# Kernel optimization log

Measured on AMD Instinct MI355X. Metric: run time of the kernel, lower is better.

The kernel has to match this reference:

```python
import jax, jax.numpy as jnp
import numpy as np

D_IN = 1024
D_OUT = 1024
SEQ = 2048
BATCH = 4


def setup_inputs() -> dict:
    key = jax.random.key(0)
    k_x, k_q, k_k, k_v = jax.random.split(key, 4)
    scale = 1.0 / np.sqrt(D_IN)  # ~ torch Linear init scale
    x = jax.random.normal(k_x, (BATCH, SEQ, D_IN), dtype=jnp.float32)
    # torch nn.Linear weights have shape [d_out, d_in]; y = x @ W.T
    Wq = jax.random.uniform(k_q, (D_OUT, D_IN), jnp.float32, -scale, scale)
    Wk = jax.random.uniform(k_k, (D_OUT, D_IN), jnp.float32, -scale, scale)
    Wv = jax.random.uniform(k_v, (D_OUT, D_IN), jnp.float32, -scale, scale)
    return {"x": x, "Wq": Wq, "Wk": Wk, "Wv": Wv}


def reference(x, Wq, Wk, Wv):
    # projections (no bias, qkv_bias=False)
    q = jnp.einsum("bsd,ed->bse", x, Wq)  # [B,S,D_OUT]
    k = jnp.einsum("bsd,ed->bse", x, Wk)
    v = jnp.einsum("bsd,ed->bse", x, Wv)
    scores = jnp.einsum("bqe,bke->bqk", q, k)  # [B,S,S]
    seq = scores.shape[-1]
    causal = jnp.tril(jnp.ones((seq, seq), dtype=bool))  # keep lower-tri
    scores = jnp.where(causal[None], scores, -jnp.inf)
    # note: original scales AFTER masking: softmax(scores / sqrt(d_k))
    inv_sqrt_dk = 1.0 / np.sqrt(k.shape[-1]).astype(np.float32)
    weights = jax.nn.softmax(scores * inv_sqrt_dk, axis=-1)
    # dropout p=0.0 (eval-equivalent): identity
    return jnp.einsum("bqk,bke->bqe", weights, v)
```

## Files before the change

### kernel.cpp

```cpp
#include <hip/hip_runtime.h>
#include <hip/hip_bf16.h>

typedef __bf16 v8bf __attribute__((ext_vector_type(8)));
typedef float v4f __attribute__((ext_vector_type(4)));

#define GBL_AS(p) ((const __attribute__((address_space(1))) unsigned int*)(p))
#define LDS_AS(p) ((__attribute__((address_space(3))) unsigned int*)(p))

__global__ void cast_f32_bf16(const float* __restrict__ src,
                              __hip_bfloat16* __restrict__ dst, int n) {
  int i = (blockIdx.x * 256 + threadIdx.x) * 4;
  if (i >= n) return;
  float4 f = *(const float4*)(src + i);
  union { __hip_bfloat16 h[4]; uint2 u; } pk;
  pk.h[0] = __float2bfloat16(f.x);
  pk.h[1] = __float2bfloat16(f.y);
  pk.h[2] = __float2bfloat16(f.z);
  pk.h[3] = __float2bfloat16(f.w);
  *(uint2*)(dst + i) = pk.u;
}

__global__ void cast_w3(const float* __restrict__ a, const float* __restrict__ b,
                        const float* __restrict__ c, __hip_bfloat16* __restrict__ dst) {
  int seg = blockIdx.x >> 10;
  const float* src = seg == 0 ? a : (seg == 1 ? b : c);
  int i = ((blockIdx.x & 1023) * 256 + threadIdx.x) * 4;
  float4 f = *(const float4*)(src + i);
  union { __hip_bfloat16 h[4]; uint2 u; } pk;
  pk.h[0] = __float2bfloat16(f.x);
  pk.h[1] = __float2bfloat16(f.y);
  pk.h[2] = __float2bfloat16(f.z);
  pk.h[3] = __float2bfloat16(f.w);
  *(uint2*)(dst + seg * 1048576 + i) = pk.u;
}

__global__ void transpose_bf16(const __hip_bfloat16* __restrict__ src,
                               __hip_bfloat16* __restrict__ dst,
                               int rows, int cols) {
  __shared__ __hip_bfloat16 t[32][33];
  long boff = (long)blockIdx.z * rows * cols;
  src += boff; dst += boff;
  int c0 = blockIdx.x * 32, r0 = blockIdx.y * 32;
  int x = threadIdx.x;
#pragma unroll
  for (int i = 0; i < 4; ++i) {
    int y = threadIdx.y + i * 8;
    t[y][x] = src[(long)(r0 + y) * cols + (c0 + x)];
  }
  __syncthreads();
#pragma unroll
  for (int i = 0; i < 4; ++i) {
    int y = threadIdx.y + i * 8;
    dst[(long)(c0 + y) * rows + (r0 + x)] = t[x][y];
  }
}

template<int MODE>
__global__ __launch_bounds__(256, 4)
void gemm_nt(const __hip_bfloat16* __restrict__ A, long sAb, int lda,
             const __hip_bfloat16* __restrict__ B, long sBb, int ldb,
             void* __restrict__ Cv, long sCb, int ldc,
             int K, float scale, float* __restrict__ sums) {
  const int tid = threadIdx.x;
  const int l = tid & 63, w = tid >> 6;
  int z, nb, mb, kend = K;
  if (MODE == 0) {
    z = blockIdx.x >> 3; nb = (blockIdx.x & 7) << 7; mb = blockIdx.y << 7;
  } else if (MODE == 1) {
    const int id = blockIdx.x;
    z = id & 3;
    const int t = id >> 2;
    int m = (int)((__builtin_sqrtf(8.0f * t + 1.0f) - 1.0f) * 0.5f);
    while ((m + 1) * (m + 2) / 2 <= t) ++m;
    while (m * (m + 1) / 2 > t) --m;
    mb = m << 7;
    nb = (t - m * (m + 1) / 2) << 7;
  } else {
    const int id = blockIdx.x;
    const int half = id >> 8, r8 = id & 255;
    const int m = r8 >> 4, low = r8 & 15;
    nb = (low >> 1) << 7;
    z = (half << 1) | (low & 1);
    const int mi = half ? (15 - m) : m;
    mb = mi << 7;
    kend = (mi + 1) << 7;
  }

  A += (long)z * sAb;
  B += (long)z * sBb;

  __shared__ alignas(16) __hip_bfloat16 As[128 * 32];
  __shared__ alignas(16) __hip_bfloat16 Bs[128 * 32];

  v4f acc[4][4] = {};
  const int wm = (w >> 1) * 64, wn = (w & 1) * 64;

  for (int k0 = 0; k0 < kend; k0 += 32) {
#pragma unroll
    for (int t = 0; t < 2; ++t) {
      const int cbase = t * 256 + w * 64;
      const int c = cbase + l;
      const int row = c >> 2, col = (c & 3) << 3;
      __builtin_amdgcn_global_load_lds(
          GBL_AS(A + (long)(mb + row) * lda + (k0 + col)),
          LDS_AS(As + cbase * 8), 16, 0, 0);
      __builtin_amdgcn_global_load_lds(
          GBL_AS(B + (long)(nb + row) * ldb + (k0 + col)),
          LDS_AS(Bs + cbase * 8), 16, 0, 0);
    }
    __syncthreads();

    v8bf af[4], bfr[4];
#pragma unroll
    for (int i = 0; i < 4; ++i) {
      af[i]  = *(const v8bf*)(As + (wm + i * 16 + (l & 15)) * 32 + ((l >> 4) << 3));
      bfr[i] = *(const v8bf*)(Bs + (wn + i * 16 + (l & 15)) * 32 + ((l >> 4) << 3));
    }
#pragma unroll
    for (int i = 0; i < 4; ++i)
#pragma unroll
      for (int j = 0; j < 4; ++j)
        acc[i][j] = __builtin_amdgcn_mfma_f32_16x16x32_bf16(af[i], bfr[j], acc[i][j], 0, 0, 0);
    __syncthreads();
  }

  const int col0 = nb + wn + (l & 15);
  const int row0 = mb + wm + ((l >> 4) << 2);
  if constexpr (MODE == 0) {
    __hip_bfloat16* C = (__hip_bfloat16*)Cv + (long)z * sCb;
#pragma unroll
    for (int i = 0; i < 4; ++i)
#pragma unroll
      for (int r = 0; r < 4; ++r) {
        long ro = (long)(row0 + i * 16 + r) * ldc;
#pragma unroll
        for (int j = 0; j < 4; ++j)
          C[ro + col0 + j * 16] = __float2bfloat16(acc[i][j][r] * scale);
      }
  } else if constexpr (MODE == 1) {
    __hip_bfloat16* C = (__hip_bfloat16*)Cv + (long)z * sCb;
    float* srow = sums + z * 2048;
#pragma unroll
    for (int i = 0; i < 4; ++i)
#pragma unroll
      for (int r = 0; r < 4; ++r) {
        const int m = row0 + i * 16 + r;
        long ro = (long)m * ldc;
        float sp = 0.f;
#pragma unroll
        for (int j = 0; j < 4; ++j) {
          const int n = col0 + j * 16;
          float p = (n <= m) ? __expf(acc[i][j][r] * scale) : 0.0f;
          sp += p;
          C[ro + n] = __float2bfloat16(p);
        }
        sp += __shfl_xor(sp, 1);
        sp += __shfl_xor(sp, 2);
        sp += __shfl_xor(sp, 4);
        sp += __shfl_xor(sp, 8);
        if ((l & 15) == 0) atomicAdd(&srow[m], sp);
      }
  } else {
    float* C = (float*)Cv + (long)z * sCb;
    const float* srow = sums + z * 2048;
#pragma unroll
    for (int i = 0; i < 4; ++i)
#pragma unroll
      for (int r = 0; r < 4; ++r) {
        const int m = row0 + i * 16 + r;
        const float s = 1.0f / srow[m];
        long ro = (long)m * ldc;
#pragma unroll
        for (int j = 0; j < 4; ++j)
          C[ro + col0 + j * 16] = acc[i][j][r] * s;
      }
  }
}

extern "C" void kernel_launch(void* const* d_in, const int* in_sizes, int n_in,
                              void* d_out, int out_size, void* d_ws, size_t ws_size,
                              hipStream_t stream) {
  const float* x  = (const float*)d_in[0];
  const float* Wq = (const float*)d_in[1];
  const float* Wk = (const float*)d_in[2];
  const float* Wv = (const float*)d_in[3];
  float* out = (float*)d_out;
  char* ws = (char*)d_ws;

  __hip_bfloat16* qkv = (__hip_bfloat16*)ws;
  __hip_bfloat16* vT  = (__hip_bfloat16*)(ws + 50331648);
  __hip_bfloat16* xb  = (__hip_bfloat16*)(ws + 67108864);
  __hip_bfloat16* Wb  = (__hip_bfloat16*)(ws + 83886080);
  __hip_bfloat16* P   = (__hip_bfloat16*)(ws + 67108864);
  float* sums         = (float*)(ws + 100663296);

  hipMemsetAsync(sums, 0, 8192 * sizeof(float), stream);

  cast_f32_bf16<<<8192, 256, 0, stream>>>(x, xb, 8388608);
  cast_w3<<<3072, 256, 0, stream>>>(Wq, Wk, Wv, Wb);

  gemm_nt<0><<<dim3(24, 64, 1), 256, 0, stream>>>(
      xb, 0L, 1024, Wb, 1048576L, 1024, qkv, 8388608L, 1024,
      1024, 1.0f, nullptr);

  transpose_bf16<<<dim3(32, 64, 4), dim3(32, 8), 0, stream>>>(
      qkv + 16777216, vT, 2048, 1024);

  gemm_nt<1><<<dim3(544, 1, 1), 256, 0, stream>>>(
      qkv, 2097152L, 1024, qkv + 8388608, 2097152L, 1024,
      P, 4194304L, 2048, 1024, 0.03125f, sums);

  gemm_nt<2><<<dim3(512, 1, 1), 256, 0, stream>>>(
      P, 4194304L, 2048, vT, 2097152L, 2048,
      out, 2097152L, 1024, 2048, 1.0f, sums);
}
```

Measured before the change: 245.2 us.

## Double-buffer LDS tiles in bf16 GEMM to overlap global loads with MFMA

The shared A/B tiles become two-stage ping-pong buffers. The next K-slice is issued via global_load_lds right after a single barrier, so the load runs while MFMAs consume the current slice, and the trailing barrier of each iteration is removed. Per-thread global row pointers are also hoisted out of the K loop. In exchange, LDS use per block doubles to 32KB, which could limit occupancy, and correctness relies on the barrier waiting for the outstanding async LDS loads.

```diff
diff --git a/kernel.cpp b/kernel.cpp
--- a/kernel.cpp
+++ b/kernel.cpp
@@ -89,40 +89,54 @@
   A += (long)z * sAb;
   B += (long)z * sBb;
 
-  __shared__ alignas(16) __hip_bfloat16 As[128 * 32];
-  __shared__ alignas(16) __hip_bfloat16 Bs[128 * 32];
+  __shared__ alignas(16) __hip_bfloat16 As[2][128 * 32];
+  __shared__ alignas(16) __hip_bfloat16 Bs[2][128 * 32];
 
   v4f acc[4][4] = {};
   const int wm = (w >> 1) * 64, wn = (w & 1) * 64;
 
+  const int cb0 = w * 64;
+  const int row0s = (cb0 + l) >> 2, col0s = ((cb0 + l) & 3) << 3;
+  const int cb1 = 256 + w * 64;
+  const int row1s = (cb1 + l) >> 2, col1s = ((cb1 + l) & 3) << 3;
+
+  const __hip_bfloat16* Arow0 = A + (long)(mb + row0s) * lda + col0s;
+  const __hip_bfloat16* Arow1 = A + (long)(mb + row1s) * lda + col1s;
+  const __hip_bfloat16* Brow0 = B + (long)(nb + row0s) * ldb + col0s;
+  const __hip_bfloat16* Brow1 = B + (long)(nb + row1s) * ldb + col1s;
+
+#define STAGE(k0, buf)                                                         \
+  do {                                                                         \
+    __builtin_amdgcn_global_load_lds(GBL_AS(Arow0 + (k0)),                     \
+        LDS_AS(&As[buf][cb0 * 8]), 16, 0, 0);                                  \
+    __builtin_amdgcn_global_load_lds(GBL_AS(Brow0 + (k0)),                     \
+        LDS_AS(&Bs[buf][cb0 * 8]), 16, 0, 0);                                  \
+    __builtin_amdgcn_global_load_lds(GBL_AS(Arow1 + (k0)),                     \
+        LDS_AS(&As[buf][cb1 * 8]), 16, 0, 0);                                  \
+    __builtin_amdgcn_global_load_lds(GBL_AS(Brow1 + (k0)),                     \
+        LDS_AS(&Bs[buf][cb1 * 8]), 16, 0, 0);                                  \
+  } while (0)
+
+  STAGE(0, 0);
+  int cur = 0;
   for (int k0 = 0; k0 < kend; k0 += 32) {
-#pragma unroll
-    for (int t = 0; t < 2; ++t) {
-      const int cbase = t * 256 + w * 64;
-      const int c = cbase + l;
-      const int row = c >> 2, col = (c & 3) << 3;
-      __builtin_amdgcn_global_load_lds(
-          GBL_AS(A + (long)(mb + row) * lda + (k0 + col)),
-          LDS_AS(As + cbase * 8), 16, 0, 0);
-      __builtin_amdgcn_global_load_lds(
-          GBL_AS(B + (long)(nb + row) * ldb + (k0 + col)),
-          LDS_AS(Bs + cbase * 8), 16, 0, 0);
-    }
     __syncthreads();
+    if (k0 + 32 < kend) STAGE(k0 + 32, cur ^ 1);
 
     v8bf af[4], bfr[4];
 #pragma unroll
     for (int i = 0; i < 4; ++i) {
-      af[i]  = *(const v8bf*)(As + (wm + i * 16 + (l & 15)) * 32 + ((l >> 4) << 3));
-      bfr[i] = *(const v8bf*)(Bs + (wn + i * 16 + (l & 15)) * 32 + ((l >> 4) << 3));
+      af[i]  = *(const v8bf*)(&As[cur][(wm + i * 16 + (l & 15)) * 32 + ((l >> 4) << 3)]);
+      bfr[i] = *(const v8bf*)(&Bs[cur][(wn + i * 16 + (l & 15)) * 32 + ((l >> 4) << 3)]);
     }
 #pragma unroll
     for (int i = 0; i < 4; ++i)
 #pragma unroll
       for (int j = 0; j < 4; ++j)
         acc[i][j] = __builtin_amdgcn_mfma_f32_16x16x32_bf16(af[i], bfr[j], acc[i][j], 0, 0, 0);
-    __syncthreads();
-  }
+    cur ^= 1;
+  }
+#undef STAGE
 
   const int col0 = nb + wn + (l & 15);
   const int row0 = mb + wm + ((l >> 4) << 2);
```

Measured after the change: 247.9 us. About the same (+1.1%).
